# Optimization experiments

Hardware: AMD Instinct MI355X
Metric: run time of the kernel (lower is better)

Reference implementation:

```python
import jax, jax.numpy as jnp
import numpy as np

D = 128  # embed dim

def linear(x, W, b):
    return x @ W.T + b

def mha1(x, w_in, b_in, w_out, b_out):
    # Single-head MultiheadAttention, x: (S, B, D), seq-first like torch.nn.MultiheadAttention
    q, k, v = jnp.split(x @ w_in.T + b_in, 3, axis=-1)
    scores = jnp.einsum('sbd,tbd->bst', q, k) / jnp.sqrt(jnp.asarray(D, x.dtype))
    att = jax.nn.softmax(scores, axis=-1)
    o = jnp.einsum('bst,tbd->sbd', att, v)
    return o @ w_out.T + b_out

def setup_inputs() -> dict:
    key = jax.random.key(0)
    ks = iter(jax.random.split(key, 32))
    def p(shape, scale=0.02):
        return (jax.random.normal(next(ks), shape, dtype=jnp.float32) * scale)
    B, S, F = 8, 2048, 3584
    inp = {
        'x': jax.random.normal(next(ks), (B, S, F), dtype=jnp.float32),
        'place_W': p((128, 2048)), 'place_b': p((128,)),
        'cast_W': p((128, 512)), 'cast_b': p((128,)),
        'action_W': p((128, 512)), 'action_b': p((128,)),
        'audio_W': p((128, 512)), 'audio_b': p((128,)),
        'e_W': p((128, 512)), 'e_b': p((128,)),
        'la_win': p((3 * D, D)), 'la_bin': p((3 * D,)),
        'la_wout': p((D, D)), 'la_bout': p((D,)),
        'be_W': p((128, 256)), 'be_b': p((128,)),
        'ba_win': p((3 * D, D)), 'ba_bin': p((3 * D,)),
        'ba_wout': p((D, D)), 'ba_bout': p((D,)),
        'bp_W': p((1, 128)), 'bp_b': p((1,)),
    }
    return inp

def reference(x, place_W, place_b, cast_W, cast_b, action_W, action_b,
              audio_W, audio_b, e_W, e_b, la_win, la_bin, la_wout, la_bout,
              be_W, be_b, ba_win, ba_bin, ba_wout, ba_bout, bp_W, bp_b):
    # --- forward_embeddings ---
    place = jax.nn.relu(linear(x[:, :, :2048], place_W, place_b))
    cast = jax.nn.relu(linear(x[:, :, 2048:2560], cast_W, cast_b))
    action = jax.nn.relu(linear(x[:, :, 2560:3072], action_W, action_b))
    audio = jax.nn.relu(linear(x[:, :, 3072:3584], audio_W, audio_b))
    feats = jnp.concatenate((place, cast, action, audio), axis=2)  # (B,S,512)
    e = jax.nn.relu(linear(feats, e_W, e_b))  # (B,S,128)
    e = jnp.transpose(e, (1, 0, 2))  # (S,B,128) seq-first
    e = mha1(e, la_win, la_bin, la_wout, la_bout)
    # --- forward_segmentation (single-pass prefix/suffix means) ---
    S = e.shape[0]
    csum = jnp.cumsum(e, axis=0)  # (S,B,D)
    total = csum[-1]
    i = jnp.arange(1, S, dtype=e.dtype)[:, None, None]
    left = csum[:-1] / i                       # mean of e[:i]
    right = (total[None] - csum[:-1]) / (S - i)  # mean of e[i:]
    cat = jnp.concatenate((left, right), axis=-1)  # (S-1,B,256)
    b = jax.nn.relu(linear(cat, be_W, be_b))
    b = mha1(b, ba_win, ba_bin, ba_wout, ba_bout)
    b = jax.nn.sigmoid(linear(b, bp_W, bp_b))[..., 0]  # (S-1,B)
    return (e, b)
```

## Files before the change

### kernel.cpp

```cpp
#include <hip/hip_runtime.h>
#include <hip/hip_bf16.h>
#include <math.h>
#include <stdint.h>


#define DEV static __device__ __forceinline__

typedef __attribute__((ext_vector_type(8))) short bf16x8;
typedef __attribute__((ext_vector_type(4))) float f32x4;

DEV uint32_t pk2bf(float a, float b) {
  __hip_bfloat162 h = __float22bfloat162_rn(make_float2(a, b));
  return *(uint32_t*)&h;
}
DEV uint2 cvt4(float4 f) {
  return make_uint2(pk2bf(f.x, f.y), pk2bf(f.z, f.w));
}
DEV uint16_t bf1(float a) { return (uint16_t)(pk2bf(a, 0.f) & 0xffffu); }
DEV float frombf(uint16_t h) {
  union { uint32_t u; float f; } v; v.u = ((uint32_t)h) << 16; return v.f;
}

#define OFF_PW      0u
#define OFF_CW      262144u
#define OFF_AW      327680u
#define OFF_UW      393216u
#define OFF_EW      458752u
#define OFF_LAWIN   524288u
#define OFF_LAWOUT  573440u
#define OFF_BEW     589824u
#define OFF_BAWIN   622592u
#define OFF_BAWOUT  671744u
#define OFF_END     688128u

struct WPtrs { const float* p[10]; };

__global__ __launch_bounds__(256) void pack_weights(WPtrs wp, uint16_t* __restrict__ WB)
{
  const uint32_t off[11] = {OFF_PW, OFF_CW, OFF_AW, OFF_UW, OFF_EW, OFF_LAWIN,
                            OFF_LAWOUT, OFF_BEW, OFF_BAWIN, OFF_BAWOUT, OFF_END};
  uint32_t h = (blockIdx.x * 256u + threadIdx.x) * 4u;
  if (h >= OFF_END) return;
  int s = 0;
  while (h >= off[s + 1]) ++s;
  float4 f = *(const float4*)(wp.p[s] + (h - off[s]));
  *(uint2*)(WB + h) = cvt4(f);
}

template<bool ABF, bool OBF, bool RELU, bool REMAP>
__global__ __launch_bounds__(256) void gemm64(
    const void* __restrict__ Ap, int lda,
    const uint16_t* __restrict__ Wb,
    const float* __restrict__ bias,
    void* __restrict__ Cp, int ldc,
    int M, int K)
{
  __shared__ __align__(16) uint16_t As[64 * 72];
  __shared__ __align__(16) uint16_t Ws[128 * 72];

  const int t  = threadIdx.x;
  const int m0 = blockIdx.x * 64;
  const int n0 = blockIdx.y * 128;
  const int w  = t >> 6, l = t & 63;
  const int ln = l & 15, qd = l >> 4;

  f32x4 acc[4][2];
#pragma unroll
  for (int i = 0; i < 4; ++i) { acc[i][0] = (f32x4){0,0,0,0}; acc[i][1] = (f32x4){0,0,0,0}; }

  const int rr = t >> 4;
  const int cl = (t & 15) * 4;
  const int r8 = t >> 3;
  const int c8 = (t & 7) * 8;

  for (int k0 = 0; k0 < K; k0 += 64) {
    __syncthreads();
    if (ABF) {
      const uint16_t* A = (const uint16_t*)Ap;
#pragma unroll
      for (int i = 0; i < 2; ++i) {
        int m = m0 + r8 + 32 * i;
        int mc = m < M ? m : M - 1;
        *(bf16x8*)(As + (size_t)(r8 + 32 * i) * 72 + c8) =
            *(const bf16x8*)(A + (size_t)mc * lda + k0 + c8);
      }
    } else {
      const float* A = (const float*)Ap;
#pragma unroll
      for (int i = 0; i < 4; ++i) {
        int m = m0 + rr + 16 * i;
        int mc = m < M ? m : M - 1;
        float4 f = *(const float4*)(A + (size_t)mc * lda + k0 + cl);
        *(uint2*)(As + (size_t)(rr + 16 * i) * 72 + cl) = cvt4(f);
      }
    }
#pragma unroll
    for (int i = 0; i < 4; ++i) {
      int n = r8 + 32 * i;
      *(bf16x8*)(Ws + (size_t)n * 72 + c8) =
          *(const bf16x8*)(Wb + (size_t)(n0 + n) * K + k0 + c8);
    }
    __syncthreads();
#pragma unroll
    for (int ks = 0; ks < 2; ++ks) {
      bf16x8 af[4], bfr[2];
#pragma unroll
      for (int mf = 0; mf < 4; ++mf)
        af[mf] = *(const bf16x8*)(As + (size_t)(mf * 16 + ln) * 72 + ks * 32 + qd * 8);
#pragma unroll
      for (int nf = 0; nf < 2; ++nf)
        bfr[nf] = *(const bf16x8*)(Ws + (size_t)(w * 32 + nf * 16 + ln) * 72 + ks * 32 + qd * 8);
#pragma unroll
      for (int mf = 0; mf < 4; ++mf)
#pragma unroll
        for (int nf = 0; nf < 2; ++nf)
          acc[mf][nf] = __builtin_amdgcn_mfma_f32_16x16x32_bf16(af[mf], bfr[nf], acc[mf][nf], 0, 0, 0);
    }
  }

#pragma unroll
  for (int mf = 0; mf < 4; ++mf) {
#pragma unroll
    for (int r = 0; r < 4; ++r) {
      int m = m0 + mf * 16 + qd * 4 + r;
      if (m < M) {
        size_t ro = REMAP ? (size_t)((m & 2047) * 8 + (m >> 11)) : (size_t)m;
#pragma unroll
        for (int nf = 0; nf < 2; ++nf) {
          int n = n0 + w * 32 + nf * 16 + ln;
          float v = acc[mf][nf][r] + bias[n];
          if (RELU) v = fmaxf(v, 0.f);
          if (OBF) ((uint16_t*)Cp)[ro * (size_t)ldc + n] = bf1(v);
          else     ((float*)Cp)[ro * (size_t)ldc + n] = v;
        }
      }
    }
  }
}

__global__ __launch_bounds__(256) void gemm_feats64(
    const float* __restrict__ x, const uint16_t* __restrict__ WB,
    const float* __restrict__ pb, const float* __restrict__ cb,
    const float* __restrict__ ab, const float* __restrict__ ub,
    uint16_t* __restrict__ feats)
{
  __shared__ __align__(16) uint16_t As[64 * 72];
  __shared__ __align__(16) uint16_t Ws[128 * 72];

  const int seg = blockIdx.y;
  const uint16_t* Wb; const float* bias; int kbase, Kseg;
  if (seg == 0)      { Wb = WB + OFF_PW; bias = pb; kbase = 0;    Kseg = 2048; }
  else if (seg == 1) { Wb = WB + OFF_CW; bias = cb; kbase = 2048; Kseg = 512; }
  else if (seg == 2) { Wb = WB + OFF_AW; bias = ab; kbase = 2560; Kseg = 512; }
  else               { Wb = WB + OFF_UW; bias = ub; kbase = 3072; Kseg = 512; }

  const int t  = threadIdx.x;
  const int m0 = blockIdx.x * 64;
  const int w  = t >> 6, l = t & 63;
  const int ln = l & 15, qd = l >> 4;

  f32x4 acc[4][2];
#pragma unroll
  for (int i = 0; i < 4; ++i) { acc[i][0] = (f32x4){0,0,0,0}; acc[i][1] = (f32x4){0,0,0,0}; }

  const int rr = t >> 4;
  const int cl = (t & 15) * 4;
  const int r8 = t >> 3;
  const int c8 = (t & 7) * 8;

  for (int k0 = 0; k0 < Kseg; k0 += 64) {
    __syncthreads();
#pragma unroll
    for (int i = 0; i < 4; ++i) {
      int m = m0 + rr + 16 * i;
      float4 f = *(const float4*)(x + (size_t)m * 3584 + kbase + k0 + cl);
      *(uint2*)(As + (size_t)(rr + 16 * i) * 72 + cl) = cvt4(f);
    }
#pragma unroll
    for (int i = 0; i < 4; ++i) {
      int n = r8 + 32 * i;
      *(bf16x8*)(Ws + (size_t)n * 72 + c8) =
          *(const bf16x8*)(Wb + (size_t)n * Kseg + k0 + c8);
    }
    __syncthreads();
#pragma unroll
    for (int ks = 0; ks < 2; ++ks) {
      bf16x8 af[4], bfr[2];
#pragma unroll
      for (int mf = 0; mf < 4; ++mf)
        af[mf] = *(const bf16x8*)(As + (size_t)(mf * 16 + ln) * 72 + ks * 32 + qd * 8);
#pragma unroll
      for (int nf = 0; nf < 2; ++nf)
        bfr[nf] = *(const bf16x8*)(Ws + (size_t)(w * 32 + nf * 16 + ln) * 72 + ks * 32 + qd * 8);
#pragma unroll
      for (int mf = 0; mf < 4; ++mf)
#pragma unroll
        for (int nf = 0; nf < 2; ++nf)
          acc[mf][nf] = __builtin_amdgcn_mfma_f32_16x16x32_bf16(af[mf], bfr[nf], acc[mf][nf], 0, 0, 0);
    }
  }

#pragma unroll
  for (int mf = 0; mf < 4; ++mf) {
#pragma unroll
    for (int r = 0; r < 4; ++r) {
      int m = m0 + mf * 16 + qd * 4 + r;
#pragma unroll
      for (int nf = 0; nf < 2; ++nf) {
        int n = w * 32 + nf * 16 + ln;
        float v = fmaxf(acc[mf][nf][r] + bias[n], 0.f);
        feats[(size_t)m * 512 + seg * 128 + n] = bf1(v);
      }
    }
  }
}

__global__ __launch_bounds__(256) void gemm_becat64(
    const float* __restrict__ csum, const float* __restrict__ part,
    const uint16_t* __restrict__ Wb, const float* __restrict__ bias,
    uint16_t* __restrict__ C)
{
  __shared__ __align__(16) uint16_t As[64 * 72];
  __shared__ __align__(16) uint16_t Ws[128 * 72];

  const int M = 16376, K = 256;
  const int t  = threadIdx.x;
  const int m0 = blockIdx.x * 64;
  const int w  = t >> 6, l = t & 63;
  const int ln = l & 15, qd = l >> 4;

  f32x4 acc[4][2];
#pragma unroll
  for (int i = 0; i < 4; ++i) { acc[i][0] = (f32x4){0,0,0,0}; acc[i][1] = (f32x4){0,0,0,0}; }

  const int rr = t >> 4;
  const int cl = (t & 15) * 4;
  const int r8 = t >> 3;
  const int c8 = (t & 7) * 8;

  for (int k0 = 0; k0 < K; k0 += 64) {
    __syncthreads();
#pragma unroll
    for (int i = 0; i < 4; ++i) {
      int m = m0 + rr + 16 * i;
      int mc = m < M ? m : M - 1;
      int j = mc >> 3, bb = mc & 7;
      int kk = k0 + cl;
      float4 f;
      if (kk < 128) {
        float4 v = *(const float4*)(csum + (size_t)mc * 128 + kk);
        float4 p = *(const float4*)(part + (size_t)(bb * 64 + (j >> 5)) * 128 + kk);
        float s = 1.f / (float)(j + 1);
        f = make_float4((v.x + p.x) * s, (v.y + p.y) * s,
                        (v.z + p.z) * s, (v.w + p.w) * s);
      } else {
        int d = kk - 128;
        float4 c0 = *(const float4*)(csum + (size_t)mc * 128 + d);
        float4 p0 = *(const float4*)(part + (size_t)(bb * 64 + (j >> 5)) * 128 + d);
        float4 ct = *(const float4*)(csum + (size_t)(16376 + bb) * 128 + d);
        float4 pt = *(const float4*)(part + (size_t)(bb * 64 + 63) * 128 + d);
        float s = 1.f / (float)(2047 - j);
        f = make_float4(((ct.x + pt.x) - (c0.x + p0.x)) * s,
                        ((ct.y + pt.y) - (c0.y + p0.y)) * s,
                        ((ct.z + pt.z) - (c0.z + p0.z)) * s,
                        ((ct.w + pt.w) - (c0.w + p0.w)) * s);
      }
      *(uint2*)(As + (size_t)(rr + 16 * i) * 72 + cl) = cvt4(f);
    }
#pragma unroll
    for (int i = 0; i < 4; ++i) {
      int n = r8 + 32 * i;
      *(bf16x8*)(Ws + (size_t)n * 72 + c8) =
          *(const bf16x8*)(Wb + (size_t)n * K + k0 + c8);
    }
    __syncthreads();
#pragma unroll
    for (int ks = 0; ks < 2; ++ks) {
      bf16x8 af[4], bfr[2];
#pragma unroll
      for (int mf = 0; mf < 4; ++mf)
        af[mf] = *(const bf16x8*)(As + (size_t)(mf * 16 + ln) * 72 + ks * 32 + qd * 8);
#pragma unroll
      for (int nf = 0; nf < 2; ++nf)
        bfr[nf] = *(const bf16x8*)(Ws + (size_t)(w * 32 + nf * 16 + ln) * 72 + ks * 32 + qd * 8);
#pragma unroll
      for (int mf = 0; mf < 4; ++mf)
#pragma unroll
        for (int nf = 0; nf < 2; ++nf)
          acc[mf][nf] = __builtin_amdgcn_mfma_f32_16x16x32_bf16(af[mf], bfr[nf], acc[mf][nf], 0, 0, 0);
    }
  }

#pragma unroll
  for (int mf = 0; mf < 4; ++mf) {
#pragma unroll
    for (int r = 0; r < 4; ++r) {
      int m = m0 + mf * 16 + qd * 4 + r;
      if (m < M) {
#pragma unroll
        for (int nf = 0; nf < 2; ++nf) {
          int n = w * 32 + nf * 16 + ln;
          C[(size_t)m * 128 + n] = bf1(fmaxf(acc[mf][nf][r] + bias[n], 0.f));
        }
      }
    }
  }
}

__global__ __launch_bounds__(256) void vpack(
    const uint16_t* __restrict__ proj, uint16_t* __restrict__ Vtb, int Slen)
{
  __shared__ __align__(16) uint16_t Vs[64][136];

  const int kt = blockIdx.x, b = blockIdx.y, t = threadIdx.x;
  const int sl = t >> 2, cg = (t & 3) * 32;
  const int s  = kt * 64 + sl;
  const int valid = s < Slen;
  const int sc = valid ? s : Slen - 1;
  const uint16_t* src = proj + ((size_t)sc * 8 + b) * 384 + 256 + cg;
#pragma unroll
  for (int i = 0; i < 4; ++i) {
    bf16x8 v;
    if (valid) v = *(const bf16x8*)(src + i * 8);
    else       v = (bf16x8){0,0,0,0,0,0,0,0};
    *(bf16x8*)(&Vs[sl][cg + i * 8]) = v;
  }
  __syncthreads();
  const int d = t >> 1, hh = t & 1;
  uint32_t wv[16];
#pragma unroll
  for (int j = 0; j < 8; ++j) {
    int k0o = hh * 8 + j;
    wv[j * 2]     = (uint32_t)Vs[k0o][d]      | ((uint32_t)Vs[k0o + 16][d] << 16);
    wv[j * 2 + 1] = (uint32_t)Vs[k0o + 32][d] | ((uint32_t)Vs[k0o + 48][d] << 16);
  }
  uint16_t* dv = Vtb + (((size_t)b * 32 + kt) * 128 + d) * 64 + hh * 32;
#pragma unroll
  for (int i = 0; i < 4; ++i)
    *(uint4*)(dv + i * 8) = *(uint4*)(&wv[i * 4]);
}

__global__ __launch_bounds__(256, 3) void attn_split3(
    const uint16_t* __restrict__ proj, const uint16_t* __restrict__ Vtb,
    float* __restrict__ Opart, float* __restrict__ ml, int Slen)
{
  __shared__ __align__(16) uint16_t KsL[64 * 136];
  __shared__ __align__(16) uint16_t VtL[128 * 72];
  __shared__ __align__(16) uint16_t PbL[4][16 * 72];

  const int t  = threadIdx.x;
  const int b  = blockIdx.y;
  const int q0 = blockIdx.x * 64;
  const int split = blockIdx.z;
  const int kbeg = split * 704;
  const int kend = (split == 2) ? Slen : kbeg + 704;
  const int w  = t >> 6;
  const int l  = t & 63;
  const int ln = l & 15;
  const int qd = l >> 4;
  const float scl = 0.08838834764831845f;

  const int kkey = t >> 2, kcg = (t & 3) * 32;
  const int vd   = t >> 1, vh  = (t & 1) * 32;

  bf16x8 qf[4];
  {
    int qrow = q0 + w * 16 + ln;
    int qc = qrow < Slen ? qrow : Slen - 1;
    const uint16_t* qp = proj + ((size_t)qc * 8 + b) * 384 + qd * 8;
#pragma unroll
    for (int ks = 0; ks < 4; ++ks) {
      union { bf16x8 v; uint16_t h[8]; uint32_t u[4]; } in, out;
      in.v = *(const bf16x8*)(qp + ks * 32);
#pragma unroll
      for (int j = 0; j < 4; ++j)
        out.u[j] = pk2bf(frombf(in.h[2 * j]) * scl, frombf(in.h[2 * j + 1]) * scl);
      qf[ks] = out.v;
    }
  }

  f32x4 oacc[8];
#pragma unroll
  for (int i = 0; i < 8; ++i) oacc[i] = (f32x4){0.f, 0.f, 0.f, 0.f};
  float mrow[4] = {-INFINITY, -INFINITY, -INFINITY, -INFINITY};
  float lrow[4] = {0.f, 0.f, 0.f, 0.f};

  const int ntiles = (kend - kbeg + 63) >> 6;

  bf16x8 kreg[4], vreg[4];
  {
    int kg = kbeg + kkey;
    int kc = kg < Slen ? kg : Slen - 1;
    const uint16_t* ksrc = proj + ((size_t)kc * 8 + b) * 384 + 128 + kcg;
#pragma unroll
    for (int i = 0; i < 4; ++i) kreg[i] = *(const bf16x8*)(ksrc + i * 8);
    const uint16_t* vsrc = Vtb + (((size_t)b * 32 + 11 * split) * 128 + vd) * 64 + vh;
#pragma unroll
    for (int i = 0; i < 4; ++i) vreg[i] = *(const bf16x8*)(vsrc + i * 8);
  }

  for (int kt = 0; kt < ntiles; ++kt) {
    __syncthreads();
    {
      uint16_t* kdst = KsL + kkey * 136 + kcg;
#pragma unroll
      for (int i = 0; i < 4; ++i) *(bf16x8*)(kdst + i * 8) = kreg[i];
      uint16_t* vdst = VtL + vd * 72 + vh;
#pragma unroll
      for (int i = 0; i < 4; ++i) *(bf16x8*)(vdst + i * 8) = vreg[i];
    }
    if (kt + 1 < ntiles) {
      int kg = kbeg + (kt + 1) * 64 + kkey;
      int kc = kg < Slen ? kg : Slen - 1;
      const uint16_t* ksrc = proj + ((size_t)kc * 8 + b) * 384 + 128 + kcg;
#pragma unroll
      for (int i = 0; i < 4; ++i) kreg[i] = *(const bf16x8*)(ksrc + i * 8);
      const int tile = 11 * split + kt + 1;
      const uint16_t* vsrc = Vtb + (((size_t)b * 32 + tile) * 128 + vd) * 64 + vh;
#pragma unroll
      for (int i = 0; i < 4; ++i) vreg[i] = *(const bf16x8*)(vsrc + i * 8);
    }
    __syncthreads();

    f32x4 sc[4];
#pragma unroll
    for (int nf = 0; nf < 4; ++nf) {
      f32x4 acc = (f32x4){0.f, 0.f, 0.f, 0.f};
#pragma unroll
      for (int ks = 0; ks < 4; ++ks) {
        bf16x8 kf = *(const bf16x8*)(KsL + (size_t)(nf * 16 + ln) * 136 + ks * 32 + qd * 8);
        acc = __builtin_amdgcn_mfma_f32_16x16x32_bf16(qf[ks], kf, acc, 0, 0, 0);
      }
      int key = kbeg + kt * 64 + nf * 16 + ln;
      if (key >= kend) { acc[0] = -1e30f; acc[1] = -1e30f; acc[2] = -1e30f; acc[3] = -1e30f; }
      sc[nf] = acc;
    }

    float alphaR[4];
#pragma unroll
    for (int r = 0; r < 4; ++r) {
      float mx = fmaxf(fmaxf(sc[0][r], sc[1][r]), fmaxf(sc[2][r], sc[3][r]));
      mx = fmaxf(mx, __shfl_xor(mx, 1));
      mx = fmaxf(mx, __shfl_xor(mx, 2));
      mx = fmaxf(mx, __shfl_xor(mx, 4));
      mx = fmaxf(mx, __shfl_xor(mx, 8));
      float mNew = fmaxf(mrow[r], mx);
      float p0 = __expf(sc[0][r] - mNew);
      float p1 = __expf(sc[1][r] - mNew);
      float p2 = __expf(sc[2][r] - mNew);
      float p3 = __expf(sc[3][r] - mNew);
      float ps = p0 + p1 + p2 + p3;
      ps += __shfl_xor(ps, 1);
      ps += __shfl_xor(ps, 2);
      ps += __shfl_xor(ps, 4);
      ps += __shfl_xor(ps, 8);
      float alpha = __expf(mrow[r] - mNew);
      mrow[r] = mNew;
      lrow[r] = lrow[r] * alpha + ps;
      alphaR[r] = alpha;
      uint2 pk;
      pk.x = pk2bf(p0, p1);
      pk.y = pk2bf(p2, p3);
      *(uint2*)(PbL[w] + (size_t)(qd * 4 + r) * 72 + ln * 4) = pk;
    }
#pragma unroll
    for (int no = 0; no < 8; ++no) {
#pragma unroll
      for (int r = 0; r < 4; ++r) oacc[no][r] *= alphaR[r];
    }
    __asm__ volatile("s_waitcnt lgkmcnt(0)" ::: "memory");

#pragma unroll
    for (int ks2 = 0; ks2 < 2; ++ks2) {
      bf16x8 af = *(const bf16x8*)(PbL[w] + (size_t)ln * 72 + ks2 * 32 + qd * 8);
#pragma unroll
      for (int no = 0; no < 8; ++no) {
        bf16x8 vf = *(const bf16x8*)(VtL + (size_t)(no * 16 + ln) * 72 + ks2 * 32 + qd * 8);
        oacc[no] = __builtin_amdgcn_mfma_f32_16x16x32_bf16(af, vf, oacc[no], 0, 0, 0);
      }
    }
  }

#pragma unroll
  for (int r = 0; r < 4; ++r) {
    int qg = q0 + w * 16 + qd * 4 + r;
    if (qg < Slen) {
      size_t row = (size_t)qg * 8 + b;
      float* dst = Opart + ((size_t)split * 16384 + row) * 128 + ln;
#pragma unroll
      for (int no = 0; no < 8; ++no) dst[no * 16] = oacc[no][r];
      if (ln == 0) {
        ml[((size_t)split * 16384 + row) * 2 + 0] = mrow[r];
        ml[((size_t)split * 16384 + row) * 2 + 1] = lrow[r];
      }
    }
  }
}

template<bool HEAD>
__global__ __launch_bounds__(256) void gemm_attc64(
    const float* __restrict__ Opart, const float* __restrict__ ml,
    const uint16_t* __restrict__ Wb,
    const float* __restrict__ bias,
    const float* __restrict__ bpW, const float* __restrict__ bpb,
    float* __restrict__ out, int M)
{
  __shared__ __align__(16) uint16_t As[64 * 72];
  __shared__ __align__(16) uint16_t Ws[128 * 72];
  __shared__ float RW[64][4];
  __shared__ float Ct[HEAD ? 64 : 1][133];

  const int K = 128;
  const int t  = threadIdx.x;
  const int m0 = blockIdx.x * 64;
  const int w  = t >> 6, l = t & 63;
  const int ln = l & 15, qd = l >> 4;

  if (t < 64) {
    int m = m0 + t;
    int mc = m < M ? m : M - 1;
    float m0v = ml[(size_t)mc * 2],                 l0 = ml[(size_t)mc * 2 + 1];
    float m1v = ml[((size_t)16384 + mc) * 2],       l1 = ml[((size_t)16384 + mc) * 2 + 1];
    float m2v = ml[((size_t)32768 + mc) * 2],       l2 = ml[((size_t)32768 + mc) * 2 + 1];
    float Mx = fmaxf(fmaxf(m0v, m1v), m2v);
    float w0 = __expf(m0v - Mx), w1 = __expf(m1v - Mx), w2 = __expf(m2v - Mx);
    RW[t][0] = w0; RW[t][1] = w1; RW[t][2] = w2;
    RW[t][3] = 1.f / (l0 * w0 + l1 * w1 + l2 * w2);
  }

  f32x4 acc[4][2];
#pragma unroll
  for (int i = 0; i < 4; ++i) { acc[i][0] = (f32x4){0,0,0,0}; acc[i][1] = (f32x4){0,0,0,0}; }

  const int rr = t >> 4;
  const int cl = (t & 15) * 4;
  const int r8 = t >> 3;
  const int c8 = (t & 7) * 8;

  for (int k0 = 0; k0 < K; k0 += 64) {
    __syncthreads();
#pragma unroll
    for (int i = 0; i < 4; ++i) {
      int m = m0 + rr + 16 * i;
      int mc = m < M ? m : M - 1;
      int kk = k0 + cl;
      float4 a = *(const float4*)(Opart + (size_t)mc * 128 + kk);
      float4 c = *(const float4*)(Opart + ((size_t)16384 + mc) * 128 + kk);
      float4 e = *(const float4*)(Opart + ((size_t)32768 + mc) * 128 + kk);
      int rl = rr + 16 * i;
      float w0 = RW[rl][0], w1 = RW[rl][1], w2 = RW[rl][2], inv = RW[rl][3];
      float4 f = make_float4((a.x * w0 + c.x * w1 + e.x * w2) * inv,
                             (a.y * w0 + c.y * w1 + e.y * w2) * inv,
                             (a.z * w0 + c.z * w1 + e.z * w2) * inv,
                             (a.w * w0 + c.w * w1 + e.w * w2) * inv);
      *(uint2*)(As + (size_t)rl * 72 + cl) = cvt4(f);
    }
#pragma unroll
    for (int i = 0; i < 4; ++i) {
      int n = r8 + 32 * i;
      *(bf16x8*)(Ws + (size_t)n * 72 + c8) =
          *(const bf16x8*)(Wb + (size_t)n * K + k0 + c8);
    }
    __syncthreads();
#pragma unroll
    for (int ks = 0; ks < 2; ++ks) {
      bf16x8 af[4], bfr[2];
#pragma unroll
      for (int mf = 0; mf < 4; ++mf)
        af[mf] = *(const bf16x8*)(As + (size_t)(mf * 16 + ln) * 72 + ks * 32 + qd * 8);
#pragma unroll
      for (int nf = 0; nf < 2; ++nf)
        bfr[nf] = *(const bf16x8*)(Ws + (size_t)(w * 32 + nf * 16 + ln) * 72 + ks * 32 + qd * 8);
#pragma unroll
      for (int mf = 0; mf < 4; ++mf)
#pragma unroll
        for (int nf = 0; nf < 2; ++nf)
          acc[mf][nf] = __builtin_amdgcn_mfma_f32_16x16x32_bf16(af[mf], bfr[nf], acc[mf][nf], 0, 0, 0);
    }
  }

  if (HEAD) {
    __syncthreads();
#pragma unroll
    for (int mf = 0; mf < 4; ++mf) {
#pragma unroll
      for (int r = 0; r < 4; ++r) {
        int rowL = mf * 16 + qd * 4 + r;
#pragma unroll
        for (int nf = 0; nf < 2; ++nf) {
          int n = w * 32 + nf * 16 + ln;
          Ct[rowL][n] = acc[mf][nf][r] + bias[n];
        }
      }
    }
    __syncthreads();
    int row = t >> 2, qg = t & 3;
    int m = m0 + row;
    float p = 0.f;
#pragma unroll
    for (int j = 0; j < 32; ++j) {
      int c = qg + j * 4;
      p += Ct[row][c] * bpW[c];
    }
    p += __shfl_xor(p, 1);
    p += __shfl_xor(p, 2);
    if (qg == 0 && m < M)
      out[m] = 1.f / (1.f + __expf(-(p + bpb[0])));
  } else {
#pragma unroll
    for (int mf = 0; mf < 4; ++mf) {
#pragma unroll
      for (int r = 0; r < 4; ++r) {
        int m = m0 + mf * 16 + qd * 4 + r;
        if (m < M) {
#pragma unroll
          for (int nf = 0; nf < 2; ++nf) {
            int n = w * 32 + nf * 16 + ln;
            out[(size_t)m * 128 + n] = acc[mf][nf][r] + bias[n];
          }
        }
      }
    }
  }
}

__global__ void cumsum_p1(const float* __restrict__ e, float* __restrict__ csum,
                          float* __restrict__ part)
{
  int chunk = blockIdx.x, b = blockIdx.y, d = threadIdx.x;
  float run = 0.f;
  int s0 = chunk * 32;
  for (int s = 0; s < 32; ++s) {
    size_t idx = ((size_t)(s0 + s) * 8 + b) * 128 + d;
    run += e[idx];
    csum[idx] = run;
  }
  part[(b * 64 + chunk) * 128 + d] = run;
}

__global__ void cumsum_p2(float* __restrict__ part)
{
  int b = blockIdx.x, d = threadIdx.x;
  float run = 0.f;
  for (int c = 0; c < 64; ++c) {
    float v = part[(b * 64 + c) * 128 + d];
    part[(b * 64 + c) * 128 + d] = run;
    run += v;
  }
}

extern "C" void kernel_launch(void* const* d_in, const int* in_sizes, int n_in,
                              void* d_out, int out_size, void* d_ws, size_t ws_size,
                              hipStream_t stream)
{
  const float* x       = (const float*)d_in[0];
  const float* pW      = (const float*)d_in[1];
  const float* pb      = (const float*)d_in[2];
  const float* cW      = (const float*)d_in[3];
  const float* cb      = (const float*)d_in[4];
  const float* aW      = (const float*)d_in[5];
  const float* ab      = (const float*)d_in[6];
  const float* uW      = (const float*)d_in[7];
  const float* ub      = (const float*)d_in[8];
  const float* eW      = (const float*)d_in[9];
  const float* eb      = (const float*)d_in[10];
  const float* la_win  = (const float*)d_in[11];
  const float* la_bin  = (const float*)d_in[12];
  const float* la_wout = (const float*)d_in[13];
  const float* la_bout = (const float*)d_in[14];
  const float* beW     = (const float*)d_in[15];
  const float* beb     = (const float*)d_in[16];
  const float* ba_win  = (const float*)d_in[17];
  const float* ba_bin  = (const float*)d_in[18];
  const float* ba_wout = (const float*)d_in[19];
  const float* ba_bout = (const float*)d_in[20];
  const float* bpW     = (const float*)d_in[21];
  const float* bpb     = (const float*)d_in[22];

  float* ws   = (float*)d_ws;
  float* outF = (float*)d_out;

  uint16_t* WB  = (uint16_t*)ws;
  float* base   = ws + 344064;
  uint16_t* featsB = (uint16_t*)base;
  float* csumB  = base;
  float* partB  = base + 2097152;
  uint16_t* eB  = (uint16_t*)(base + 4194304);
  uint16_t* projB = (uint16_t*)(base + 5242880);
  uint16_t* VtbB  = (uint16_t*)(base + 8388608);
  float* OpartB = base + 9437184;
  float* mlB    = base + 15728640;

  WPtrs wp;
  wp.p[0] = pW; wp.p[1] = cW; wp.p[2] = aW; wp.p[3] = uW; wp.p[4] = eW;
  wp.p[5] = la_win; wp.p[6] = la_wout; wp.p[7] = beW; wp.p[8] = ba_win; wp.p[9] = ba_wout;
  pack_weights<<<dim3(672), 256, 0, stream>>>(wp, WB);

  gemm_feats64<<<dim3(256, 4), 256, 0, stream>>>(x, WB, pb, cb, ab, ub, featsB);
  gemm64<true, true, true, true><<<dim3(256, 1), 256, 0, stream>>>(
      featsB, 512, WB + OFF_EW, eb, eB, 128, 16384, 512);
  gemm64<true, true, false, false><<<dim3(256, 3), 256, 0, stream>>>(
      eB, 128, WB + OFF_LAWIN, la_bin, projB, 384, 16384, 128);
  vpack<<<dim3(32, 8), 256, 0, stream>>>(projB, VtbB, 2048);
  attn_split3<<<dim3(32, 8, 3), 256, 0, stream>>>(projB, VtbB, OpartB, mlB, 2048);
  gemm_attc64<false><<<dim3(256), 256, 0, stream>>>(
      OpartB, mlB, WB + OFF_LAWOUT, la_bout, nullptr, nullptr, outF, 16384);
  cumsum_p1<<<dim3(64, 8), 128, 0, stream>>>(outF, csumB, partB);
  cumsum_p2<<<dim3(8), 128, 0, stream>>>(partB);
  gemm_becat64<<<dim3(256), 256, 0, stream>>>(csumB, partB, WB + OFF_BEW, beb, eB);
  gemm64<true, true, false, false><<<dim3(256, 3), 256, 0, stream>>>(
      eB, 128, WB + OFF_BAWIN, ba_bin, projB, 384, 16376, 128);
  vpack<<<dim3(32, 8), 256, 0, stream>>>(projB, VtbB, 2047);
  attn_split3<<<dim3(32, 8, 3), 256, 0, stream>>>(projB, VtbB, OpartB, mlB, 2047);
  gemm_attc64<true><<<dim3(256), 256, 0, stream>>>(
      OpartB, mlB, WB + OFF_BAWOUT, ba_bout, bpW, bpb, outF + 2097152, 16376);
}
```

Baseline: 537.2 us.

## Compute transposed scores so P stays in registers, dropping LDS round-trip

The QK^T MFMA swaps its operands, so each lane holds scores for one query row across keys. P can then be packed straight into bf16 MFMA A-operands instead of going through a per-warp LDS buffer. The V pack kernel reorders keys to match this register layout. Row max and sum now need only two cross-lane shuffles and one softmax state per lane, with the alpha values sent back to output rows by shuffle. This removes LDS writes and reads, a waitcnt, and some shuffles, but depends on the key permutation being exactly right.

```diff
diff --git a/kernel.cpp b/kernel.cpp
--- a/kernel.cpp
+++ b/kernel.cpp
@@ -316,8 +316,8 @@
   const int sl = t >> 2, cg = (t & 3) * 32;
   const int s  = kt * 64 + sl;
   const int valid = s < Slen;
-  const int sc = valid ? s : Slen - 1;
-  const uint16_t* src = proj + ((size_t)sc * 8 + b) * 384 + 256 + cg;
+  const int sc2 = valid ? s : Slen - 1;
+  const uint16_t* src = proj + ((size_t)sc2 * 8 + b) * 384 + 256 + cg;
 #pragma unroll
   for (int i = 0; i < 4; ++i) {
     bf16x8 v;
@@ -329,10 +329,9 @@
   const int d = t >> 1, hh = t & 1;
   uint32_t wv[16];
 #pragma unroll
-  for (int j = 0; j < 8; ++j) {
-    int k0o = hh * 8 + j;
-    wv[j * 2]     = (uint32_t)Vs[k0o][d]      | ((uint32_t)Vs[k0o + 16][d] << 16);
-    wv[j * 2 + 1] = (uint32_t)Vs[k0o + 32][d] | ((uint32_t)Vs[k0o + 48][d] << 16);
+  for (int i = 0; i < 16; ++i) {
+    int K = 32 * hh + 16 * ((i >> 1) & 1) + 4 * ((i >> 2) & 3) + 2 * (i & 1);
+    wv[i] = (uint32_t)Vs[K][d] | ((uint32_t)Vs[K + 1][d] << 16);
   }
   uint16_t* dv = Vtb + (((size_t)b * 32 + kt) * 128 + d) * 64 + hh * 32;
 #pragma unroll
@@ -346,7 +345,6 @@
 {
   __shared__ __align__(16) uint16_t KsL[64 * 136];
   __shared__ __align__(16) uint16_t VtL[128 * 72];
-  __shared__ __align__(16) uint16_t PbL[4][16 * 72];
 
   const int t  = threadIdx.x;
   const int b  = blockIdx.y;
@@ -382,8 +380,8 @@
   f32x4 oacc[8];
 #pragma unroll
   for (int i = 0; i < 8; ++i) oacc[i] = (f32x4){0.f, 0.f, 0.f, 0.f};
-  float mrow[4] = {-INFINITY, -INFINITY, -INFINITY, -INFINITY};
-  float lrow[4] = {0.f, 0.f, 0.f, 0.f};
+  float mrow = -INFINITY;
+  float lrow = 0.f;
 
   const int ntiles = (kend - kbeg + 63) >> 6;
 
@@ -422,62 +420,72 @@
     }
     __syncthreads();
 
-    f32x4 sc[4];
+    float sc[4][4];
 #pragma unroll
     for (int nf = 0; nf < 4; ++nf) {
       f32x4 acc = (f32x4){0.f, 0.f, 0.f, 0.f};
 #pragma unroll
       for (int ks = 0; ks < 4; ++ks) {
         bf16x8 kf = *(const bf16x8*)(KsL + (size_t)(nf * 16 + ln) * 136 + ks * 32 + qd * 8);
-        acc = __builtin_amdgcn_mfma_f32_16x16x32_bf16(qf[ks], kf, acc, 0, 0, 0);
-      }
-      int key = kbeg + kt * 64 + nf * 16 + ln;
-      if (key >= kend) { acc[0] = -1e30f; acc[1] = -1e30f; acc[2] = -1e30f; acc[3] = -1e30f; }
-      sc[nf] = acc;
-    }
+        acc = __builtin_amdgcn_mfma_f32_16x16x32_bf16(kf, qf[ks], acc, 0, 0, 0);
+      }
+      int keyb = kbeg + kt * 64 + nf * 16 + qd * 4;
+#pragma unroll
+      for (int r = 0; r < 4; ++r)
+        sc[nf][r] = (keyb + r < kend) ? acc[r] : -1e30f;
+    }
+
+    float mx = sc[0][0];
+#pragma unroll
+    for (int nf = 0; nf < 4; ++nf)
+#pragma unroll
+      for (int r = 0; r < 4; ++r) mx = fmaxf(mx, sc[nf][r]);
+    mx = fmaxf(mx, __shfl_xor(mx, 16));
+    mx = fmaxf(mx, __shfl_xor(mx, 32));
+    float mNew = fmaxf(mrow, mx);
+
+    float ps = 0.f;
+#pragma unroll
+    for (int nf = 0; nf < 4; ++nf) {
+      float p0 = __expf(sc[nf][0] - mNew);
+      float p1 = __expf(sc[nf][1] - mNew);
+      float p2 = __expf(sc[nf][2] - mNew);
+      float p3 = __expf(sc[nf][3] - mNew);
+      sc[nf][0] = p0; sc[nf][1] = p1; sc[nf][2] = p2; sc[nf][3] = p3;
+      ps += (p0 + p1) + (p2 + p3);
+    }
+    ps += __shfl_xor(ps, 16);
+    ps += __shfl_xor(ps, 32);
+
+    float alpha = __expf(mrow - mNew);
+    mrow = mNew;
+    lrow = lrow * alpha + ps;
 
     float alphaR[4];
 #pragma unroll
-    for (int r = 0; r < 4; ++r) {
-      float mx = fmaxf(fmaxf(sc[0][r], sc[1][r]), fmaxf(sc[2][r], sc[3][r]));
-      mx = fmaxf(mx, __shfl_xor(mx, 1));
-      mx = fmaxf(mx, __shfl_xor(mx, 2));
-      mx = fmaxf(mx, __shfl_xor(mx, 4));
-      mx = fmaxf(mx, __shfl_xor(mx, 8));
-      float mNew = fmaxf(mrow[r], mx);
-      float p0 = __expf(sc[0][r] - mNew);
-      float p1 = __expf(sc[1][r] - mNew);
-      float p2 = __expf(sc[2][r] - mNew);
-      float p3 = __expf(sc[3][r] - mNew);
-      float ps = p0 + p1 + p2 + p3;
-      ps += __shfl_xor(ps, 1);
-      ps += __shfl_xor(ps, 2);
-      ps += __shfl_xor(ps, 4);
-      ps += __shfl_xor(ps, 8);
-      float alpha = __expf(mrow[r] - mNew);
-      mrow[r] = mNew;
-      lrow[r] = lrow[r] * alpha + ps;
-      alphaR[r] = alpha;
-      uint2 pk;
-      pk.x = pk2bf(p0, p1);
-      pk.y = pk2bf(p2, p3);
-      *(uint2*)(PbL[w] + (size_t)(qd * 4 + r) * 72 + ln * 4) = pk;
-    }
+    for (int r = 0; r < 4; ++r)
+      alphaR[r] = __shfl(alpha, (l & 48) | (qd * 4 + r));
 #pragma unroll
     for (int no = 0; no < 8; ++no) {
 #pragma unroll
       for (int r = 0; r < 4; ++r) oacc[no][r] *= alphaR[r];
     }
-    __asm__ volatile("s_waitcnt lgkmcnt(0)" ::: "memory");
-
-#pragma unroll
-    for (int ks2 = 0; ks2 < 2; ++ks2) {
-      bf16x8 af = *(const bf16x8*)(PbL[w] + (size_t)ln * 72 + ks2 * 32 + qd * 8);
-#pragma unroll
-      for (int no = 0; no < 8; ++no) {
-        bf16x8 vf = *(const bf16x8*)(VtL + (size_t)(no * 16 + ln) * 72 + ks2 * 32 + qd * 8);
-        oacc[no] = __builtin_amdgcn_mfma_f32_16x16x32_bf16(af, vf, oacc[no], 0, 0, 0);
-      }
+
+    union { bf16x8 v; uint32_t u[4]; } pa0, pa1;
+#pragma unroll
+    for (int i = 0; i < 4; ++i) {
+      pa0.u[i] = pk2bf(sc[(i >> 1)][(i & 1) * 2],     sc[(i >> 1)][(i & 1) * 2 + 1]);
+      pa1.u[i] = pk2bf(sc[2 + (i >> 1)][(i & 1) * 2], sc[2 + (i >> 1)][(i & 1) * 2 + 1]);
+    }
+#pragma unroll
+    for (int no = 0; no < 8; ++no) {
+      bf16x8 vf = *(const bf16x8*)(VtL + (size_t)(no * 16 + ln) * 72 + qd * 8);
+      oacc[no] = __builtin_amdgcn_mfma_f32_16x16x32_bf16(pa0.v, vf, oacc[no], 0, 0, 0);
+    }
+#pragma unroll
+    for (int no = 0; no < 8; ++no) {
+      bf16x8 vf = *(const bf16x8*)(VtL + (size_t)(no * 16 + ln) * 72 + 32 + qd * 8);
+      oacc[no] = __builtin_amdgcn_mfma_f32_16x16x32_bf16(pa1.v, vf, oacc[no], 0, 0, 0);
     }
   }
 
@@ -489,10 +497,14 @@
       float* dst = Opart + ((size_t)split * 16384 + row) * 128 + ln;
 #pragma unroll
       for (int no = 0; no < 8; ++no) dst[no * 16] = oacc[no][r];
-      if (ln == 0) {
-        ml[((size_t)split * 16384 + row) * 2 + 0] = mrow[r];
-        ml[((size_t)split * 16384 + row) * 2 + 1] = lrow[r];
-      }
+    }
+  }
+  {
+    int qg = q0 + w * 16 + ln;
+    if (qd == 0 && qg < Slen) {
+      size_t row = (size_t)qg * 8 + b;
+      ml[((size_t)split * 16384 + row) * 2 + 0] = mrow;
+      ml[((size_t)split * 16384 + row) * 2 + 1] = lrow;
     }
   }
 }
```

Result: faster. 519.3 us (-3.3%).
